# Kernel optimization log

Hardware: AMD Instinct MI355X
Metric: run time of the kernel (lower is better)

Reference implementation:

```python
import jax, jax.numpy as jnp
import numpy as np

L = 2            # decoder layers (layer slice)
H = 1024         # hidden size
NH = 16          # attention heads
HD = 64          # head dim
NKV = 4          # kv heads (GQA)
KVD = NKV * HD   # 256
I = 2816         # intermediate size
V = 32000        # vocab
R = 64           # lora rank
S = 512          # seq len
B = 1            # batch
BLK = 64         # quantization block size
NCODE = 16       # 2**k codebook entries (k=4)
LORA_S = 16.0 / 64.0  # lora_alpha / lora_r
EPS = 1e-6
THETA = 10000.0


def _dequant(idx2d, am, codebook):
    # blockwise k-bit dequant: w[i] = codebook[idx[i]] * absmax[i // BLK]
    n, k = idx2d.shape
    w = codebook[idx2d.reshape(-1)].reshape(-1, BLK) * am[:, None]
    return w.reshape(n, k)


def _linear(x, idx, am, codebook, A, Bm):
    # fused dequant-matmul + low-rank LoRA update
    w = _dequant(idx, am, codebook)           # [N, K]
    return x @ w.T + LORA_S * ((x @ A.T) @ Bm.T)


def _rmsnorm(x, w):
    return x * jax.lax.rsqrt(jnp.mean(x * x, axis=-1, keepdims=True) + EPS) * w


def _rope_cache():
    inv_freq = 1.0 / (THETA ** (np.arange(0, HD, 2, dtype=np.float32) / HD))
    freqs = np.outer(np.arange(S, dtype=np.float32), inv_freq)
    emb = np.concatenate([freqs, freqs], axis=-1)  # [S, HD]
    return jnp.asarray(np.cos(emb)), jnp.asarray(np.sin(emb))


def _apply_rope(x, cos, sin):
    # x: [B, S, n_heads, HD]; llama-style non-interleaved rotate_half
    x1, x2 = jnp.split(x, 2, axis=-1)
    rot = jnp.concatenate([-x2, x1], axis=-1)
    return x * cos[None, :, None, :] + rot * sin[None, :, None, :]


def _forward(input_ids, embed, codebook, q_idx, q_am, qA, qB, k_idx, k_am, kA, kB,
             v_idx, v_am, vA, vB, o_idx, o_am, oA, oB, g_idx, g_am, gA, gB,
             u_idx, u_am, uA, uB, d_idx, d_am, dA, dB, ln1, ln2, final_norm,
             lm_idx, lm_am):
    cos, sin = _rope_cache()
    mask = jnp.tril(jnp.ones((S, S), dtype=bool))
    h = embed[input_ids]  # [B, S, H]
    for i in range(L):
        # --- attention block ---
        x = _rmsnorm(h, ln1[i])
        q = _linear(x, q_idx[i], q_am[i], codebook, qA[i], qB[i]).reshape(B, S, NH, HD)
        k = _linear(x, k_idx[i], k_am[i], codebook, kA[i], kB[i]).reshape(B, S, NKV, HD)
        v = _linear(x, v_idx[i], v_am[i], codebook, vA[i], vB[i]).reshape(B, S, NKV, HD)
        q = _apply_rope(q, cos, sin)
        k = _apply_rope(k, cos, sin)
        k = jnp.repeat(k, NH // NKV, axis=2)  # GQA expand
        v = jnp.repeat(v, NH // NKV, axis=2)
        scores = jnp.einsum('bqhd,bkhd->bhqk', q, k) / np.float32(np.sqrt(HD))
        scores = jnp.where(mask[None, None], scores, jnp.float32(-1e30))
        attn = jax.nn.softmax(scores, axis=-1)
        ctx = jnp.einsum('bhqk,bkhd->bqhd', attn, v).reshape(B, S, H)
        h = h + _linear(ctx, o_idx[i], o_am[i], codebook, oA[i], oB[i])
        # --- SwiGLU MLP block ---
        x = _rmsnorm(h, ln2[i])
        gate = _linear(x, g_idx[i], g_am[i], codebook, gA[i], gB[i])
        up = _linear(x, u_idx[i], u_am[i], codebook, uA[i], uB[i])
        h = h + _linear(jax.nn.silu(gate) * up, d_idx[i], d_am[i], codebook, dA[i], dB[i])
    h = _rmsnorm(h, final_norm)
    logits = h @ _dequant(lm_idx, lm_am, codebook).T  # quantized lm_head, no LoRA
    return logits


def setup_inputs():
    key = jax.random.key(0)
    keys = iter(jax.random.split(key, 80))
    def idx(shape):
        return jax.random.randint(next(keys), shape, 0, NCODE, dtype=jnp.int32)
    def amL(nblocks):
        return jax.random.uniform(next(keys), (L, nblocks), dtype=jnp.float32) * 0.02 + 1e-3
    def lora(shape):
        return jax.random.normal(next(keys), shape, dtype=jnp.float32) * 0.02
    inp = {}
    inp['input_ids'] = jax.random.randint(next(keys), (B, S), 0, V, dtype=jnp.int32)
    inp['embed'] = jax.random.normal(next(keys), (V, H), dtype=jnp.float32) * 0.02
    inp['codebook'] = jnp.linspace(-1.0, 1.0, NCODE, dtype=jnp.float32)
    inp['q_idx'] = idx((L, H, H));    inp['q_am'] = amL(H * H // BLK)
    inp['qA'] = lora((L, R, H));      inp['qB'] = lora((L, H, R))
    inp['k_idx'] = idx((L, KVD, H));  inp['k_am'] = amL(KVD * H // BLK)
    inp['kA'] = lora((L, R, H));      inp['kB'] = lora((L, KVD, R))
    inp['v_idx'] = idx((L, KVD, H));  inp['v_am'] = amL(KVD * H // BLK)
    inp['vA'] = lora((L, R, H));      inp['vB'] = lora((L, KVD, R))
    inp['o_idx'] = idx((L, H, H));    inp['o_am'] = amL(H * H // BLK)
    inp['oA'] = lora((L, R, H));      inp['oB'] = lora((L, H, R))
    inp['g_idx'] = idx((L, I, H));    inp['g_am'] = amL(I * H // BLK)
    inp['gA'] = lora((L, R, H));      inp['gB'] = lora((L, I, R))
    inp['u_idx'] = idx((L, I, H));    inp['u_am'] = amL(I * H // BLK)
    inp['uA'] = lora((L, R, H));      inp['uB'] = lora((L, I, R))
    inp['d_idx'] = idx((L, H, I));    inp['d_am'] = amL(H * I // BLK)
    inp['dA'] = lora((L, R, I));      inp['dB'] = lora((L, H, R))
    inp['ln1'] = jnp.ones((L, H), dtype=jnp.float32)
    inp['ln2'] = jnp.ones((L, H), dtype=jnp.float32)
    inp['final_norm'] = jnp.ones((H,), dtype=jnp.float32)
    inp['lm_idx'] = idx((V, H))
    inp['lm_am'] = jax.random.uniform(next(keys), (V * H // BLK,), dtype=jnp.float32) * 0.02 + 1e-3
    return inp


def reference(input_ids, embed, codebook, q_idx, q_am, qA, qB, k_idx, k_am, kA, kB,
              v_idx, v_am, vA, vB, o_idx, o_am, oA, oB, g_idx, g_am, gA, gB,
              u_idx, u_am, uA, uB, d_idx, d_am, dA, dB, ln1, ln2, final_norm,
              lm_idx, lm_am):
    return _forward(input_ids, embed, codebook, q_idx, q_am, qA, qB, k_idx, k_am, kA, kB,
                    v_idx, v_am, vA, vB, o_idx, o_am, oA, oB, g_idx, g_am, gA, gB,
                    u_idx, u_am, uA, uB, d_idx, d_am, dA, dB, ln1, ln2, final_norm,
                    lm_idx, lm_am)
```

## Files before the change

kernel.cpp:

```cpp
#include <hip/hip_runtime.h>
#include <math.h>

constexpr int LAYERS = 2;
constexpr int H      = 1024;
constexpr int NH     = 16;
constexpr int HD     = 64;
constexpr int NKV    = 4;
constexpr int KVD    = 256;
constexpr int IDIM   = 2816;
constexpr int VOCAB  = 32000;
constexpr int RR     = 64;
constexpr int SEQ    = 512;
constexpr float LORA_SCALE = 0.25f;
constexpr float RMS_EPS    = 1e-6f;

typedef __attribute__((ext_vector_type(8))) __bf16 bf16x8;
typedef __attribute__((ext_vector_type(4))) __bf16 bf16x4;
typedef __attribute__((ext_vector_type(4))) float f32x4;

__device__ __forceinline__ float dot4(float4 a, float4 b) {
    return a.x*b.x + a.y*b.y + a.z*b.z + a.w*b.w;
}

__device__ __forceinline__ bf16x8 pack8(float4 a, float4 b) {
    bf16x8 p;
    p[0] = (__bf16)a.x; p[1] = (__bf16)a.y; p[2] = (__bf16)a.z; p[3] = (__bf16)a.w;
    p[4] = (__bf16)b.x; p[5] = (__bf16)b.y; p[6] = (__bf16)b.z; p[7] = (__bf16)b.w;
    return p;
}

__device__ __forceinline__ bf16x8 dq8a(int4 a, int4 b, float sa, float ba) {
    bf16x8 p;
    p[0] = (__bf16)fmaf((float)a.x, sa, ba); p[1] = (__bf16)fmaf((float)a.y, sa, ba);
    p[2] = (__bf16)fmaf((float)a.z, sa, ba); p[3] = (__bf16)fmaf((float)a.w, sa, ba);
    p[4] = (__bf16)fmaf((float)b.x, sa, ba); p[5] = (__bf16)fmaf((float)b.y, sa, ba);
    p[6] = (__bf16)fmaf((float)b.z, sa, ba); p[7] = (__bf16)fmaf((float)b.w, sa, ba);
    return p;
}

__global__ __launch_bounds__(256) void k_embed(const int* __restrict__ ids,
                                               const float* __restrict__ embed,
                                               float* __restrict__ h) {
    int s = blockIdx.x;
    int t = threadIdx.x;
    const float4* src = (const float4*)(embed + (size_t)ids[s] * H);
    float4* dst = (float4*)(h + (size_t)s * H);
    dst[t] = src[t];
}

__global__ __launch_bounds__(256) void k_rmsnorm(const float* __restrict__ h,
                                                 const float* __restrict__ w,
                                                 __bf16* __restrict__ x) {
    __shared__ float red[4];
    int s = blockIdx.x, t = threadIdx.x;
    float4 a = ((const float4*)(h + (size_t)s * H))[t];
    float ss = a.x*a.x + a.y*a.y + a.z*a.z + a.w*a.w;
    #pragma unroll
    for (int o = 32; o > 0; o >>= 1) ss += __shfl_xor(ss, o, 64);
    if ((t & 63) == 0) red[t >> 6] = ss;
    __syncthreads();
    float tot = red[0] + red[1] + red[2] + red[3];
    float scale = rsqrtf(tot * (1.0f / H) + RMS_EPS);
    float4 wv = ((const float4*)w)[t];
    bf16x4 o4;
    o4[0] = (__bf16)(a.x*scale*wv.x); o4[1] = (__bf16)(a.y*scale*wv.y);
    o4[2] = (__bf16)(a.z*scale*wv.z); o4[3] = (__bf16)(a.w*scale*wv.w);
    *(bf16x4*)&x[(size_t)s * H + t * 4] = o4;
}

struct GSeg {
    const int* widx; const float* am; const float* lA; const float* lB;
    float* y; int N; int ntiles;
};

template<int NSEG, bool LORA, int EPI, int KSPLIT>
__global__ __launch_bounds__(256) void k_gemm(
    const __bf16* __restrict__ x, const float* __restrict__ cb,
    GSeg s0, GSeg s1, GSeg s2, int K, int ntTotal, __bf16* __restrict__ y2)
{
    __shared__ __align__(16) __bf16 As[2][128][64];
    __shared__ __align__(16) __bf16 Bs[2][128][64];
    __shared__ __align__(16) __bf16 La[LORA ? 2 : 1][LORA ? 64 : 1][64];

    const int id = blockIdx.x + (blockIdx.y << 2);
    const int mtile = (id >> 3) & 3;
    int n = ((id >> 5) << 3) + (id & 7);
    if (n >= ntTotal) return;

    const int* widx; const float* am; const float* lA; const float* lB;
    float* y; int N;
    if (NSEG == 1 || n < s0.ntiles) {
        widx=s0.widx; am=s0.am; lA=s0.lA; lB=s0.lB; y=s0.y; N=s0.N;
    } else if (NSEG == 2 || (n - s0.ntiles) < s1.ntiles) {
        n -= s0.ntiles;
        widx=s1.widx; am=s1.am; lA=s1.lA; lB=s1.lB; y=s1.y; N=s1.N;
    } else {
        n -= s0.ntiles + s1.ntiles;
        widx=s2.widx; am=s2.am; lA=s2.lA; lB=s2.lB; y=s2.y; N=s2.N;
    }
    const int sbase = mtile * 128;
    const int nbase = n * 128;
    const int t    = threadIdx.x;
    const int lane = t & 63;
    const int wave = t >> 6;
    const int wm = (wave >> 1) * 64;
    const int wn = (wave & 1) * 64;
    const float cb0  = cb[0];
    const float cbsl = (cb[15] - cb[0]) * (1.0f / 15.0f);
    const int srow = t >> 3;
    const int scol = (t & 7) * 8;
    const int wsw  = (srow & 7) << 3;
    const int rsw  = (lane & 7) << 3;
    const int KB   = K >> 6;

    int kbLo, kbHi;
    if constexpr (KSPLIT > 1) {
        kbLo = ((int)blockIdx.z * KB) / KSPLIT;
        kbHi = (((int)blockIdx.z + 1) * KB) / KSPLIT;
    } else { kbLo = 0; kbHi = KB; }

    f32x4 acc[4][4];
    f32x4 accl[4][4];
    const f32x4 fz = {0.f, 0.f, 0.f, 0.f};
    #pragma unroll
    for (int i = 0; i < 4; ++i)
        #pragma unroll
        for (int j = 0; j < 4; ++j) { acc[i][j] = fz; if constexpr (LORA) accl[i][j] = fz; }

    bf16x8 pa[4]; int4 pi0[4], pi1[4]; float pam[4];
    float4 pl0[2], pl1[2];
    auto LOADT = [&](int kb_) {
        const int k0_ = kb_ << 6;
        #pragma unroll
        for (int p = 0; p < 4; ++p) {
            const int row_ = p * 32 + srow;
            pa[p] = *(const bf16x8*)&x[(size_t)(sbase + row_) * K + k0_ + scol];
            const int* ip_ = &widx[(size_t)(nbase + row_) * K + k0_ + scol];
            pi0[p] = ((const int4*)ip_)[0];
            pi1[p] = ((const int4*)ip_)[1];
            pam[p] = am[(size_t)(nbase + row_) * KB + kb_];
        }
        if constexpr (LORA) {
            #pragma unroll
            for (int p = 0; p < 2; ++p) {
                const float* lp = &lA[(size_t)(p * 32 + srow) * K + k0_ + scol];
                pl0[p] = *(const float4*)lp;
                pl1[p] = *(const float4*)(lp + 4);
            }
        }
    };
    auto STAGE = [&](int wb) {
        #pragma unroll
        for (int p = 0; p < 4; ++p) {
            int row = p * 32 + srow;
            *(bf16x8*)&As[wb][row][scol ^ wsw] = pa[p];
            float sa = cbsl * pam[p], ba = cb0 * pam[p];
            *(bf16x8*)&Bs[wb][row][scol ^ wsw] = dq8a(pi0[p], pi1[p], sa, ba);
        }
        if constexpr (LORA) {
            #pragma unroll
            for (int p = 0; p < 2; ++p)
                *(bf16x8*)&La[wb][p * 32 + srow][scol ^ wsw] = pack8(pl0[p], pl1[p]);
        }
    };

    LOADT(kbLo);
    STAGE(0);
    if (kbLo + 1 < kbHi) LOADT(kbLo + 1);
    __syncthreads();

    int cur = 0;
    for (int kb = kbLo; kb < kbHi; ++kb, cur ^= 1) {
        #pragma unroll
        for (int s = 0; s < 2; ++s) {
            bf16x8 a[4], b[4];
            #pragma unroll
            for (int mi = 0; mi < 4; ++mi)
                a[mi] = *(bf16x8*)&As[cur][wm + mi*16 + (lane & 15)][(s*32 + (lane >> 4)*8) ^ rsw];
            #pragma unroll
            for (int ni = 0; ni < 4; ++ni)
                b[ni] = *(bf16x8*)&Bs[cur][wn + ni*16 + (lane & 15)][(s*32 + (lane >> 4)*8) ^ rsw];
            #pragma unroll
            for (int mi = 0; mi < 4; ++mi)
                #pragma unroll
                for (int ni = 0; ni < 4; ++ni)
                    acc[mi][ni] = __builtin_amdgcn_mfma_f32_16x16x32_bf16(
                        a[mi], b[ni], acc[mi][ni], 0, 0, 0);
            if constexpr (LORA) {
                bf16x8 bl[4];
                #pragma unroll
                for (int ni = 0; ni < 4; ++ni)
                    bl[ni] = *(bf16x8*)&La[cur][ni*16 + (lane & 15)][(s*32 + (lane >> 4)*8) ^ rsw];
                #pragma unroll
                for (int mi = 0; mi < 4; ++mi)
                    #pragma unroll
                    for (int ni = 0; ni < 4; ++ni)
                        accl[mi][ni] = __builtin_amdgcn_mfma_f32_16x16x32_bf16(
                            a[mi], bl[ni], accl[mi][ni], 0, 0, 0);
            }
        }
        if (kb + 1 < kbHi) {
            STAGE(cur ^ 1);
            if (kb + 2 < kbHi) LOADT(kb + 2);
        }
        __syncthreads();
    }

    if constexpr (LORA) {
        if (wn == 0) {
            const int cr = (lane >> 4) * 4, cc = lane & 15;
            #pragma unroll
            for (int mi = 0; mi < 4; ++mi)
                #pragma unroll
                for (int ni = 0; ni < 4; ++ni)
                    #pragma unroll
                    for (int r = 0; r < 4; ++r) {
                        int row = wm + mi*16 + cr + r;
                        As[0][row][(ni*16 + cc) ^ ((row & 7) << 3)] =
                            (__bf16)(LORA_SCALE * accl[mi][ni][r]);
                    }
        }
        #pragma unroll
        for (int p = 0; p < 4; ++p) {
            int row = p * 32 + srow;
            const float* bp = &lB[(size_t)(nbase + row) * RR + scol];
            *(bf16x8*)&Bs[0][row][scol ^ wsw] = pack8(*(const float4*)bp, *(const float4*)(bp + 4));
        }
        __syncthreads();
        #pragma unroll
        for (int s = 0; s < 2; ++s) {
            bf16x8 a[4], b[4];
            #pragma unroll
            for (int mi = 0; mi < 4; ++mi)
                a[mi] = *(bf16x8*)&As[0][wm + mi*16 + (lane & 15)][(s*32 + (lane >> 4)*8) ^ rsw];
            #pragma unroll
            for (int ni = 0; ni < 4; ++ni)
                b[ni] = *(bf16x8*)&Bs[0][wn + ni*16 + (lane & 15)][(s*32 + (lane >> 4)*8) ^ rsw];
            #pragma unroll
            for (int mi = 0; mi < 4; ++mi)
                #pragma unroll
                for (int ni = 0; ni < 4; ++ni)
                    acc[mi][ni] = __builtin_amdgcn_mfma_f32_16x16x32_bf16(
                        a[mi], b[ni], acc[mi][ni], 0, 0, 0);
        }
    }

    const int cr = (lane >> 4) * 4;
    const int cc = lane & 15;
    #pragma unroll
    for (int mi = 0; mi < 4; ++mi) {
        #pragma unroll
        for (int ni = 0; ni < 4; ++ni) {
            int gr = sbase + wm + mi * 16 + cr;
            int gc = nbase + wn + ni * 16 + cc;
            #pragma unroll
            for (int r = 0; r < 4; ++r) {
                size_t off = (size_t)(gr + r) * N + gc;
                if constexpr (EPI == 0) {
                    if constexpr (KSPLIT > 1) atomicAdd(&y[off], acc[mi][ni][r]);
                    else                      y[off] = acc[mi][ni][r];
                }
                if constexpr (EPI == 1) {
                    if constexpr (KSPLIT > 1) atomicAdd(&y[off], acc[mi][ni][r]);
                    else                      y[off] += acc[mi][ni][r];
                }
            }
        }
    }
    (void)y2;
}

__global__ __launch_bounds__(256) void k_silu(const float* __restrict__ g,
                                              const float* __restrict__ u,
                                              __bf16* __restrict__ out, int n4) {
    int i = blockIdx.x * 256 + threadIdx.x;
    int stride = gridDim.x * 256;
    for (; i < n4; i += stride) {
        float4 gv = ((const float4*)g)[i];
        float4 uv = ((const float4*)u)[i];
        bf16x4 o4;
        o4[0] = (__bf16)(gv.x / (1.f + __expf(-gv.x)) * uv.x);
        o4[1] = (__bf16)(gv.y / (1.f + __expf(-gv.y)) * uv.y);
        o4[2] = (__bf16)(gv.z / (1.f + __expf(-gv.z)) * uv.z);
        o4[3] = (__bf16)(gv.w / (1.f + __expf(-gv.w)) * uv.w);
        *(bf16x4*)&out[(size_t)i * 4] = o4;
    }
}

__global__ __launch_bounds__(256) void k_rope(float* __restrict__ q, float* __restrict__ k) {
    int s  = blockIdx.x;
    int hs = blockIdx.y * 4 + (threadIdx.x >> 6);
    int d  = threadIdx.x & 63;
    float* p = (hs < NH) ? q + ((size_t)s * NH + hs) * HD
                         : k + ((size_t)s * NKV + (hs - NH)) * HD;
    int j = d & 31;
    float inv = exp2f(-(float)(2 * j) * (13.287712379549449f / 64.0f));
    float ang = (float)s * inv;
    float sn, c;
    __sincosf(ang, &sn, &c);
    float xv = p[d];
    float other = (d < 32) ? -p[d + 32] : p[d - 32];
    p[d] = xv * c + other * sn;
}

__global__ __launch_bounds__(256) void k_scores(const float* __restrict__ q,
                                                const float* __restrict__ k,
                                                float* __restrict__ attn) {
    int qt = blockIdx.x;
    int h  = blockIdx.y;
    int kvh = h >> 2;
    __shared__ float qs[16][68];
    __shared__ float ks[64][68];
    __shared__ float sc[16][528];
    int t = threadIdx.x;
    { int row = t >> 4; int c4 = (t & 15) << 2;
      *(float4*)&qs[row][c4] = *(const float4*)&q[(size_t)(qt*16 + row) * H + h * HD + c4]; }
    const int cmax = (qt * 16 + 15) >> 6;
    for (int c = 0; c <= cmax; ++c) {
        #pragma unroll
        for (int i = 0; i < 4; ++i) {
            int id = t + i * 256; int row = id >> 4; int c4 = (id & 15) << 2;
            *(float4*)&ks[row][c4] = *(const float4*)&k[(size_t)(c*64 + row) * KVD + kvh * HD + c4];
        }
        __syncthreads();
        int r  = t >> 4;
        int cc = (t & 15) << 2;
        float4 acc = make_float4(0.f, 0.f, 0.f, 0.f);
        #pragma unroll
        for (int kk = 0; kk < 64; kk += 4) {
            float4 a = *(const float4*)&qs[r][kk];
            acc.x += dot4(a, *(const float4*)&ks[cc + 0][kk]);
            acc.y += dot4(a, *(const float4*)&ks[cc + 1][kk]);
            acc.z += dot4(a, *(const float4*)&ks[cc + 2][kk]);
            acc.w += dot4(a, *(const float4*)&ks[cc + 3][kk]);
        }
        acc.x *= 0.125f; acc.y *= 0.125f; acc.z *= 0.125f; acc.w *= 0.125f;
        *(float4*)&sc[r][c * 64 + cc] = acc;
        __syncthreads();
    }
    int r = t >> 4, lane = t & 15;
    int qpos = qt * 16 + r;
    float mx = -1e30f;
    for (int c = lane; c <= qpos; c += 16) mx = fmaxf(mx, sc[r][c]);
    #pragma unroll
    for (int o = 8; o > 0; o >>= 1) mx = fmaxf(mx, __shfl_xor(mx, o, 16));
    float sum = 0.f;
    for (int c = lane; c <= qpos; c += 16) {
        float e = __expf(sc[r][c] - mx);
        sc[r][c] = e; sum += e;
    }
    #pragma unroll
    for (int o = 8; o > 0; o >>= 1) sum += __shfl_xor(sum, o, 16);
    float inv = 1.0f / sum;
    for (int c = lane; c < SEQ; c += 16)
        attn[((size_t)h * SEQ + qpos) * SEQ + c] = (c <= qpos) ? sc[r][c] * inv : 0.f;
}

__global__ __launch_bounds__(256) void k_ctx(const float* __restrict__ attn,
                                             const float* __restrict__ v,
                                             __bf16* __restrict__ ctx) {
    int qt = blockIdx.x, h = blockIdx.y, kvh = h >> 2;
    __shared__ float as_[16][68];
    __shared__ float vs[64][68];
    int t = threadIdx.x;
    int row = t >> 4;
    int col = (t & 15) * 4;
    float acc0 = 0.f, acc1 = 0.f, acc2 = 0.f, acc3 = 0.f;
    const int cmax = (qt * 16 + 15) >> 6;
    for (int c = 0; c <= cmax; ++c) {
        { int r2 = t >> 4; int c4 = (t & 15) << 2;
          *(float4*)&as_[r2][c4] = *(const float4*)&attn[((size_t)h*SEQ + qt*16 + r2) * SEQ + c*64 + c4]; }
        #pragma unroll
        for (int i = 0; i < 4; ++i) {
            int id = t + i * 256; int r2 = id >> 4; int c4 = (id & 15) << 2;
            *(float4*)&vs[r2][c4] = *(const float4*)&v[(size_t)(c*64 + r2) * KVD + kvh * HD + c4];
        }
        __syncthreads();
        #pragma unroll 16
        for (int kk = 0; kk < 64; ++kk) {
            float a = as_[row][kk];
            float4 b = *(const float4*)&vs[kk][col];
            acc0 += a * b.x; acc1 += a * b.y; acc2 += a * b.z; acc3 += a * b.w;
        }
        __syncthreads();
    }
    bf16x4 o4;
    o4[0] = (__bf16)acc0; o4[1] = (__bf16)acc1;
    o4[2] = (__bf16)acc2; o4[3] = (__bf16)acc3;
    *(bf16x4*)&ctx[(size_t)(qt*16 + row) * H + h * HD + col] = o4;
}

extern "C" void kernel_launch(void* const* d_in, const int* in_sizes, int n_in,
                              void* d_out, int out_size, void* d_ws, size_t ws_size,
                              hipStream_t stream) {
    const int*   p_ids   = (const int*)  d_in[0];
    const float* p_embed = (const float*)d_in[1];
    const float* p_cb    = (const float*)d_in[2];
    const int*   p_qidx  = (const int*)  d_in[3];  const float* p_qam = (const float*)d_in[4];
    const float* p_qA    = (const float*)d_in[5];  const float* p_qB  = (const float*)d_in[6];
    const int*   p_kidx  = (const int*)  d_in[7];  const float* p_kam = (const float*)d_in[8];
    const float* p_kA    = (const float*)d_in[9];  const float* p_kB  = (const float*)d_in[10];
    const int*   p_vidx  = (const int*)  d_in[11]; const float* p_vam = (const float*)d_in[12];
    const float* p_vA    = (const float*)d_in[13]; const float* p_vB  = (const float*)d_in[14];
    const int*   p_oidx  = (const int*)  d_in[15]; const float* p_oam = (const float*)d_in[16];
    const float* p_oA    = (const float*)d_in[17]; const float* p_oB  = (const float*)d_in[18];
    const int*   p_gidx  = (const int*)  d_in[19]; const float* p_gam = (const float*)d_in[20];
    const float* p_gA    = (const float*)d_in[21]; const float* p_gB  = (const float*)d_in[22];
    const int*   p_uidx  = (const int*)  d_in[23]; const float* p_uam = (const float*)d_in[24];
    const float* p_uA    = (const float*)d_in[25]; const float* p_uB  = (const float*)d_in[26];
    const int*   p_didx  = (const int*)  d_in[27]; const float* p_dam = (const float*)d_in[28];
    const float* p_dA    = (const float*)d_in[29]; const float* p_dB  = (const float*)d_in[30];
    const float* p_ln1   = (const float*)d_in[31];
    const float* p_ln2   = (const float*)d_in[32];
    const float* p_fn    = (const float*)d_in[33];
    const int*   p_lmidx = (const int*)  d_in[34]; const float* p_lmam = (const float*)d_in[35];

    char* w = (char*)d_ws;
    const size_t MB = 1024 * 1024;
    float*  hbuf  = (float*) (w + 0);
    __bf16* xb16  = (__bf16*)(w + 2*MB);
    float*  qb    = (float*) (w + 3*MB);
    float*  kb    = (float*) (w + 5*MB);
    float*  vb    = (float*) (w + 5*MB + 512*1024);
    __bf16* ctx16 = (__bf16*)(w + 6*MB);
    float*  attn  = (float*) (w + 7*MB);
    __bf16* g16   = (__bf16*)(w + 7*MB);
    float*  gatef = (float*) (w + 11*MB);
    float*  upf   = gatef + (size_t)SEQ*IDIM;

    const GSeg znull = {nullptr, nullptr, nullptr, nullptr, nullptr, 0, 0};
    const size_t mlpB = (size_t)SEQ * IDIM * sizeof(float);

    k_embed<<<SEQ, 256, 0, stream>>>(p_ids, p_embed, hbuf);

    for (int l = 0; l < LAYERS; ++l) {
        const int*   qi  = p_qidx + (size_t)l * H * H;      const float* qa = p_qam + (size_t)l * (H*H/64);
        const float* qAl = p_qA + (size_t)l * RR * H;       const float* qBl = p_qB + (size_t)l * H * RR;
        const int*   ki  = p_kidx + (size_t)l * KVD * H;    const float* ka = p_kam + (size_t)l * (KVD*H/64);
        const float* kAl = p_kA + (size_t)l * RR * H;       const float* kBl = p_kB + (size_t)l * KVD * RR;
        const int*   vi  = p_vidx + (size_t)l * KVD * H;    const float* va = p_vam + (size_t)l * (KVD*H/64);
        const float* vAl = p_vA + (size_t)l * RR * H;       const float* vBl = p_vB + (size_t)l * KVD * RR;
        const int*   oi  = p_oidx + (size_t)l * H * H;      const float* oa = p_oam + (size_t)l * (H*H/64);
        const float* oAl = p_oA + (size_t)l * RR * H;       const float* oBl = p_oB + (size_t)l * H * RR;
        const int*   gi  = p_gidx + (size_t)l * IDIM * H;   const float* ga = p_gam + (size_t)l * (IDIM*H/64);
        const float* gAl = p_gA + (size_t)l * RR * H;       const float* gBl = p_gB + (size_t)l * IDIM * RR;
        const int*   ui  = p_uidx + (size_t)l * IDIM * H;   const float* ua = p_uam + (size_t)l * (IDIM*H/64);
        const float* uAl = p_uA + (size_t)l * RR * H;       const float* uBl = p_uB + (size_t)l * IDIM * RR;
        const int*   di  = p_didx + (size_t)l * H * IDIM;   const float* da = p_dam + (size_t)l * (H*IDIM/64);
        const float* dAl = p_dA + (size_t)l * RR * IDIM;    const float* dBl = p_dB + (size_t)l * H * RR;

        k_rmsnorm<<<SEQ, 256, 0, stream>>>(hbuf, p_ln1 + (size_t)l * H, xb16);
        hipMemsetAsync(qb, 0, 3*MB, stream);
        {
            GSeg sq = {qi, qa, qAl, qBl, qb, H,   8};
            GSeg sk = {ki, ka, kAl, kBl, kb, KVD, 2};
            GSeg sv = {vi, va, vAl, vBl, vb, KVD, 2};
            k_gemm<3,true,0,8><<<dim3(4,16,8), 256, 0, stream>>>(
                xb16, p_cb, sq, sk, sv, H, 12, nullptr);
        }
        k_rope<<<dim3(SEQ, 5), 256, 0, stream>>>(qb, kb);
        k_scores<<<dim3(SEQ/16, NH), 256, 0, stream>>>(qb, kb, attn);
        k_ctx<<<dim3(SEQ/16, NH), 256, 0, stream>>>(attn, vb, ctx16);
        {
            GSeg so = {oi, oa, oAl, oBl, hbuf, H, 8};
            k_gemm<1,true,1,8><<<dim3(4,8,8), 256, 0, stream>>>(
                ctx16, p_cb, so, znull, znull, H, 8, nullptr);
        }

        k_rmsnorm<<<SEQ, 256, 0, stream>>>(hbuf, p_ln2 + (size_t)l * H, xb16);
        hipMemsetAsync(gatef, 0, 2 * mlpB, stream);
        {
            GSeg sg = {gi, ga, gAl, gBl, gatef, IDIM, 22};
            GSeg su = {ui, ua, uAl, uBl, upf,   IDIM, 22};
            k_gemm<2,true,0,4><<<dim3(4,48,4), 256, 0, stream>>>(
                xb16, p_cb, sg, su, znull, H, 44, nullptr);
        }
        k_silu<<<1024, 256, 0, stream>>>(gatef, upf, g16, SEQ * IDIM / 4);
        {
            GSeg sd = {di, da, dAl, dBl, hbuf, H, 8};
            k_gemm<1,true,1,11><<<dim3(4,8,11), 256, 0, stream>>>(
                g16, p_cb, sd, znull, znull, IDIM, 8, nullptr);
        }
    }

    k_rmsnorm<<<SEQ, 256, 0, stream>>>(hbuf, p_fn, xb16);
    {
        GSeg sl = {p_lmidx, p_lmam, nullptr, nullptr, (float*)d_out, VOCAB, 250};
        k_gemm<1,false,0,1><<<dim3(4,256), 256, 0, stream>>>(
            xb16, p_cb, sl, znull, znull, H, 250, nullptr);
    }
}
```

Before: 898.5 us.

## Add LDS-free register-direct LM-head kernel and shorten GEMM prefetch distance

Replaces the generic shared-memory GEMM for the LM head with a dedicated kernel. Each wave loads its x fragments and quantized weight indices straight from global memory into registers and dequantizes them in place, with no LDS staging and no barriers. Separately, the generic GEMM's register prefetch now issues the next tile's loads at the top of each iteration rather than two tiles ahead, which reduces live registers but hides less latency. The LM-head kernel has no explicit prefetch, so global load latency is exposed, and weights are reloaded per wave instead of being shared through LDS.

```diff
diff --git a/kernel.cpp b/kernel.cpp
--- a/kernel.cpp
+++ b/kernel.cpp
@@ -166,11 +166,11 @@
 
     LOADT(kbLo);
     STAGE(0);
-    if (kbLo + 1 < kbHi) LOADT(kbLo + 1);
     __syncthreads();
 
     int cur = 0;
     for (int kb = kbLo; kb < kbHi; ++kb, cur ^= 1) {
+        if (kb + 1 < kbHi) LOADT(kb + 1);
         #pragma unroll
         for (int s = 0; s < 2; ++s) {
             bf16x8 a[4], b[4];
@@ -199,10 +199,7 @@
                             a[mi], bl[ni], accl[mi][ni], 0, 0, 0);
             }
         }
-        if (kb + 1 < kbHi) {
-            STAGE(cur ^ 1);
-            if (kb + 2 < kbHi) LOADT(kb + 2);
-        }
+        if (kb + 1 < kbHi) STAGE(cur ^ 1);
         __syncthreads();
     }
 
@@ -268,6 +265,94 @@
         }
     }
     (void)y2;
+}
+
+__global__ __launch_bounds__(256) void k_lmhead(
+    const __bf16* __restrict__ x, const float* __restrict__ cb,
+    const int* __restrict__ widx, const float* __restrict__ am,
+    float* __restrict__ y)
+{
+    constexpr int K  = H;
+    constexpr int KB = K >> 6;
+    constexpr int NT = VOCAB / 128;
+
+    const int id = blockIdx.x + (blockIdx.y << 2);
+    const int mtile = (id >> 3) & 3;
+    int n = ((id >> 5) << 3) + (id & 7);
+    if (n >= NT) return;
+
+    const int sbase = mtile * 128;
+    const int nbase = n * 128;
+    const int t    = threadIdx.x;
+    const int lane = t & 63;
+    const int wave = t >> 6;
+    const int wm = (wave >> 1) * 64;
+    const int wn = (wave & 1) * 64;
+    const int fr = lane & 15;
+    const int fk = (lane >> 4) * 8;
+    const float cb0  = cb[0];
+    const float cbsl = (cb[15] - cb[0]) * (1.0f / 15.0f);
+
+    const __bf16* xrow[4];
+    const int*    wrow[4];
+    const float*  arow[4];
+    #pragma unroll
+    for (int mi = 0; mi < 4; ++mi)
+        xrow[mi] = &x[(size_t)(sbase + wm + mi*16 + fr) * K + fk];
+    #pragma unroll
+    for (int ni = 0; ni < 4; ++ni) {
+        int r = nbase + wn + ni*16 + fr;
+        wrow[ni] = &widx[(size_t)r * K + fk];
+        arow[ni] = &am[(size_t)r * KB];
+    }
+
+    f32x4 acc[4][4];
+    const f32x4 fz = {0.f, 0.f, 0.f, 0.f};
+    #pragma unroll
+    for (int i = 0; i < 4; ++i)
+        #pragma unroll
+        for (int j = 0; j < 4; ++j) acc[i][j] = fz;
+
+    for (int kb = 0; kb < KB; ++kb) {
+        const int k0 = kb << 6;
+        float amv[4];
+        #pragma unroll
+        for (int ni = 0; ni < 4; ++ni) amv[ni] = arow[ni][kb];
+        #pragma unroll
+        for (int s = 0; s < 2; ++s) {
+            bf16x8 a[4], b[4];
+            #pragma unroll
+            for (int mi = 0; mi < 4; ++mi)
+                a[mi] = *(const bf16x8*)&xrow[mi][k0 + s*32];
+            #pragma unroll
+            for (int ni = 0; ni < 4; ++ni) {
+                const int* ip = &wrow[ni][k0 + s*32];
+                int4 i0 = ((const int4*)ip)[0];
+                int4 i1 = ((const int4*)ip)[1];
+                b[ni] = dq8a(i0, i1, cbsl * amv[ni], cb0 * amv[ni]);
+            }
+            #pragma unroll
+            for (int mi = 0; mi < 4; ++mi)
+                #pragma unroll
+                for (int ni = 0; ni < 4; ++ni)
+                    acc[mi][ni] = __builtin_amdgcn_mfma_f32_16x16x32_bf16(
+                        a[mi], b[ni], acc[mi][ni], 0, 0, 0);
+        }
+    }
+
+    const int cr = (lane >> 4) * 4;
+    const int cc = lane & 15;
+    #pragma unroll
+    for (int mi = 0; mi < 4; ++mi) {
+        #pragma unroll
+        for (int ni = 0; ni < 4; ++ni) {
+            int gr = sbase + wm + mi * 16 + cr;
+            int gc = nbase + wn + ni * 16 + cc;
+            #pragma unroll
+            for (int r = 0; r < 4; ++r)
+                y[(size_t)(gr + r) * VOCAB + gc] = acc[mi][ni][r];
+        }
+    }
 }
 
 __global__ __launch_bounds__(256) void k_silu(const float* __restrict__ g,
@@ -484,9 +569,6 @@
     }
 
     k_rmsnorm<<<SEQ, 256, 0, stream>>>(hbuf, p_fn, xb16);
-    {
-        GSeg sl = {p_lmidx, p_lmam, nullptr, nullptr, (float*)d_out, VOCAB, 250};
-        k_gemm<1,false,0,1><<<dim3(4,256), 256, 0, stream>>>(
-            xb16, p_cb, sl, znull, znull, H, 250, nullptr);
-    }
-}
+    k_lmhead<<<dim3(4,256), 256, 0, stream>>>(
+        xb16, p_cb, p_lmidx, p_lmam, (float*)d_out);
+}
```

After: 1.009 ms. +12.3%, slower.
